# Kernel optimization log

Hardware: AMD Instinct MI355X
Metric: run time of the kernel (lower is better)

Reference implementation:

```python
import jax, jax.numpy as jnp
import numpy as np


def setup_inputs() -> dict:
    key = jax.random.key(0)
    k1, k2 = jax.random.split(key)
    B, D = 8192, 256
    pred = jax.random.normal(k1, (B, D), dtype=jnp.float32)
    gt = jax.random.normal(k2, (B, D), dtype=jnp.float32)
    sigma = jnp.ones((), dtype=jnp.float32)  # learned scalar param (dim=1, mode='auto')
    return {"pred": pred, "gt": gt, "sigma": sigma}


def reference(pred, gt, sigma):
    # p, g: [B, D] (flatten from start_dim=1 is identity for 2D inputs)
    p = pred.reshape(pred.shape[0], -1)
    g = gt.reshape(gt.shape[0], -1)
    B, D = p.shape
    noise_var = sigma ** 2
    # MVN(mean=p_i, cov=noise_var*I).log_prob(g_j) in closed form:
    # -0.5 * ||g_j - p_i||^2 / noise_var - 0.5 * D * log(2*pi*noise_var)
    sq_dist = (
        jnp.sum(p * p, axis=-1)[:, None]
        + jnp.sum(g * g, axis=-1)[None, :]
        - 2.0 * (p @ g.T)
    )  # [B, B]
    log_norm = 0.5 * D * jnp.log(2.0 * jnp.pi * noise_var)
    logits = -0.5 * sq_dist / noise_var - log_norm  # [B, B], class dim = 1
    # cross_entropy(logits, arange(B)) = mean_i(-log_softmax(logits)[i, i])
    logp = jax.nn.log_softmax(logits, axis=1)
    loss = -jnp.mean(jnp.diagonal(logp))
    loss = loss * jax.lax.stop_gradient(2.0 * noise_var)
    return loss
```

## Files before the change

kernel.cpp:

```cpp
#include <hip/hip_runtime.h>
#include <hip/hip_fp8.h>


typedef float f32x4 __attribute__((ext_vector_type(4)));
typedef long llong2 __attribute__((ext_vector_type(2)));

#define LN2F 0.6931471805599453f
#define LOG2EF 1.4426950408889634f
#define NB 8192
#define ND 256
#define NCHUNK 32

#define AS1 __attribute__((address_space(1)))
#define AS3 __attribute__((address_space(3)))

__device__ __forceinline__ float fexp2(float x) {
#if __has_builtin(__builtin_amdgcn_exp2f)
  return __builtin_amdgcn_exp2f(x);
#else
  float r;
  asm("v_exp_f32 %0, %1\n\ts_nop 1" : "=v"(r) : "v"(x));
  return r;
#endif
}

__device__ __forceinline__ int pack4_fp8(float a, float b, float c, float d) {
#if __has_builtin(__builtin_amdgcn_cvt_pk_fp8_f32)
  int w = __builtin_amdgcn_cvt_pk_fp8_f32(a, b, 0, false);
  w = __builtin_amdgcn_cvt_pk_fp8_f32(c, d, w, true);
  return w;
#else
  unsigned b0 = __hip_fp8_e4m3(a).__x, b1 = __hip_fp8_e4m3(b).__x;
  unsigned b2 = __hip_fp8_e4m3(c).__x, b3 = __hip_fp8_e4m3(d).__x;
  return (int)(b0 | (b1 << 8) | (b2 << 16) | (b3 << 24));
#endif
}

__global__ __launch_bounds__(256) void vmse_prep(
    const float* __restrict__ pred, const float* __restrict__ gt,
    const float* __restrict__ sigma,
    unsigned char* __restrict__ Ah, unsigned char* __restrict__ Bh,
    float* __restrict__ diag, float* __restrict__ gnorm,
    float* __restrict__ ghs)
{
  const float nv = sigma[0] * sigma[0];
  const float s = LOG2EF / nv;
  const int row = blockIdx.x * 4 + (threadIdx.x >> 6);
  const int l = threadIdx.x & 63;
  const float4 p = *(const float4*)(pred + row * ND + l * 4);
  const float4 g = *(const float4*)(gt   + row * ND + l * 4);
  const int pw = pack4_fp8(p.x * s, p.y * s, p.z * s, p.w * s);
  const int gw = pack4_fp8(g.x, g.y, g.z, g.w);
  const int pos = (l >> 4) * 64 + ((l & 7) >> 1) * 16 + ((l >> 3) & 1) * 8 + (l & 1) * 4;
  *(int*)(Ah + row * ND + pos) = pw;
  *(int*)(Bh + row * ND + pos) = gw;
  float dd = p.x * g.x + p.y * g.y + p.z * g.z + p.w * g.w;
  float gg = g.x * g.x + g.y * g.y + g.z * g.z + g.w * g.w;
  #pragma unroll
  for (int off = 1; off < 64; off <<= 1) {
    dd += __shfl_xor(dd, off);
    gg += __shfl_xor(gg, off);
  }
  if (l == 0) {
    diag[row] = dd;
    gnorm[row] = gg;
    ghs[row] = -0.5f * s * gg;
  }
}

__device__ __forceinline__ void epi(const f32x4 z, float& m, float& l) {
  const float tmax = fmaxf(fmaxf(z[0], z[1]), fmaxf(z[2], z[3]));
  if (__any(tmax > m + 8.0f)) {
    const float nm = fmaxf(m, tmax);
    l *= fexp2(m - nm);
    m = nm;
  }
  l += (fexp2(z[0] - m) + fexp2(z[1] - m)) + (fexp2(z[2] - m) + fexp2(z[3] - m));
}

__global__ __launch_bounds__(256, 4) void vmse_main(
    const unsigned char* __restrict__ Ah, const unsigned char* __restrict__ Bh,
    const float* __restrict__ ghs, float* __restrict__ partial)
{
  __shared__ unsigned char lds[2][32 * 256];
  __shared__ float lds_ghs[256];
  const int tid = threadIdx.x;
  const int lane = tid & 63;
  const int wid = tid >> 6;
  const int rb = blockIdx.x & 63;
  const int ch = blockIdx.x >> 6;
  const int r15 = lane & 15;
  const int hi = lane >> 4;
  const int j0 = ch * 256;

  long pf[2][8];
  #pragma unroll
  for (int ns = 0; ns < 2; ++ns) {
    const unsigned char* prow =
        Ah + (size_t)((rb * 128) + (wid * 32) + (ns * 16) + r15) * ND;
    #pragma unroll
    for (int kk2 = 0; kk2 < 4; ++kk2) {
      const llong2 v = *(const llong2*)(prow + kk2 * 64 + hi * 16);
      pf[ns][2 * kk2] = v[0];
      pf[ns][2 * kk2 + 1] = v[1];
    }
  }

  lds_ghs[tid] = ghs[j0 + tid];

  const int r7 = r15 & 7;
  const int r7lo = r7 & 3, r7hi = r7 >> 2;
  const int h2 = hi ^ r7lo;
  const char* base = (const char*)&lds[0][0] + r15 * 256 + h2 * 16;
  const char* pE = base + r7hi * 64;
  const char* pO = base + 64 - r7hi * 64;

  const unsigned char* srcb[2];
  #pragma unroll
  for (int i = 0; i < 2; ++i) {
    const int q = wid * 2 + i;
    const int r = q * 4 + (lane >> 4);
    const int cg = (lane & 15) ^ (r & 7);
    srcb[i] = Bh + (size_t)(j0 + r) * ND + cg * 16;
  }

  #define STAGE(buf, t)                                                      \
    {                                                                        \
      _Pragma("unroll")                                                      \
      for (int i = 0; i < 2; ++i)                                            \
        __builtin_amdgcn_global_load_lds(                                    \
            (const AS1 unsigned int*)(srcb[i] + (t) * 8192),                 \
            (AS3 unsigned int*)&lds[buf][(wid * 2 + i) * 1024], 16, 0, 0);   \
    }

  float m2[2], l2[2];
  #pragma unroll
  for (int ns = 0; ns < 2; ++ns) { m2[ns] = -3.0e38f; l2[ns] = 0.0f; }

  #define COMPUTE(PE, PO, gp)                                                \
    {                                                                        \
      _Pragma("unroll")                                                      \
      for (int ms = 0; ms < 2; ++ms) {                                       \
        const f32x4 gv = *(const f32x4*)((gp) + ms * 64 + hi * 16);          \
        f32x4 a0 = gv;                                                       \
        f32x4 a1 = gv;                                                       \
        const llong2 gA = *(const llong2*)((PE) + ms * 4096);                \
        const llong2 gB = *(const llong2*)((PO) + ms * 4096);                \
        const llong2 gC = *(const llong2*)((PE) + ms * 4096 + 128);          \
        const llong2 gD = *(const llong2*)((PO) + ms * 4096 + 128);          \
        const long gf[8] = {gA[0], gA[1], gB[0], gB[1],                      \
                            gC[0], gC[1], gD[0], gD[1]};                     \
        __builtin_amdgcn_s_setprio(1);                                       \
        _Pragma("unroll")                                                    \
        for (int kk = 0; kk < 8; ++kk) {                                     \
          a0 = __builtin_amdgcn_mfma_f32_16x16x32_fp8_fp8(gf[kk], pf[0][kk], a0, 0, 0, 0); \
          a1 = __builtin_amdgcn_mfma_f32_16x16x32_fp8_fp8(gf[kk], pf[1][kk], a1, 0, 0, 0); \
        }                                                                    \
        __builtin_amdgcn_s_setprio(0);                                       \
        epi(a0, m2[0], l2[0]);                                               \
        epi(a1, m2[1], l2[1]);                                               \
      }                                                                      \
    }

  STAGE(0, 0);
  __syncthreads();

  const char* gp = (const char*)lds_ghs;
  for (int tt = 0; tt < 4; ++tt) {
    const int t = 2 * tt;
    STAGE(1, t + 1);
    COMPUTE(pE, pO, gp);
    gp += 128;
    __syncthreads();
    if (t + 2 < 8) STAGE(0, t + 2);
    COMPUTE(pE + 8192, pO + 8192, gp);
    gp += 128;
    __syncthreads();
  }

  #pragma unroll
  for (int ns = 0; ns < 2; ++ns) {
    float m = m2[ns], l = l2[ns];
    #pragma unroll
    for (int off = 16; off <= 32; off <<= 1) {
      const float om = __shfl_xor(m, off);
      const float ol = __shfl_xor(l, off);
      const float nm = fmaxf(m, om);
      l = l * fexp2(m - nm) + ol * fexp2(om - nm);
      m = nm;
    }
    if (hi == 0) {
      const int row = rb * 128 + wid * 32 + ns * 16 + r15;
      partial[row * NCHUNK + ch] = m + log2f(l);
    }
  }
}

__global__ __launch_bounds__(256) void vmse_combine(
    const float* __restrict__ partial, const float* __restrict__ diag,
    const float* __restrict__ gnorm, const float* __restrict__ sigma,
    float* __restrict__ bsum)
{
  const int r = blockIdx.x * 256 + threadIdx.x;
  const float nv = sigma[0] * sigma[0];
  float p[NCHUNK];
  float M = -3.0e38f;
  #pragma unroll
  for (int c = 0; c < NCHUNK; ++c) { p[c] = partial[r * NCHUNK + c]; M = fmaxf(M, p[c]); }
  float ssum = 0.f;
  #pragma unroll
  for (int c = 0; c < NCHUNK; ++c) ssum += exp2f(p[c] - M);
  const float lse2 = M + log2f(ssum);
  const float zii = (diag[r] - 0.5f * gnorm[r]) / nv;
  float contrib = LN2F * lse2 - zii;
  #pragma unroll
  for (int off = 1; off < 64; off <<= 1) contrib += __shfl_xor(contrib, off);
  __shared__ float wsum[4];
  if ((threadIdx.x & 63) == 0) wsum[threadIdx.x >> 6] = contrib;
  __syncthreads();
  if (threadIdx.x == 0)
    bsum[blockIdx.x] = (wsum[0] + wsum[1]) + (wsum[2] + wsum[3]);
}

__global__ __launch_bounds__(64) void vmse_final(
    const float* __restrict__ bsum, const float* __restrict__ sigma,
    float* __restrict__ out)
{
  const int lane = threadIdx.x;
  float v = (lane < 32) ? bsum[lane] : 0.f;
  #pragma unroll
  for (int off = 1; off < 64; off <<= 1) v += __shfl_xor(v, off);
  if (lane == 0) {
    const float nv = sigma[0] * sigma[0];
    out[0] = v * (2.0f * nv / (float)NB);
  }
}

extern "C" void kernel_launch(void* const* d_in, const int* in_sizes, int n_in,
                              void* d_out, int out_size, void* d_ws, size_t ws_size,
                              hipStream_t stream)
{
  const float* pred  = (const float*)d_in[0];
  const float* gt    = (const float*)d_in[1];
  const float* sigma = (const float*)d_in[2];
  char* ws = (char*)d_ws;
  unsigned char* Ah = (unsigned char*)(ws);
  unsigned char* Bh = (unsigned char*)(ws + (2u << 20));
  float* gnorm   = (float*)(ws + (4u << 20));
  float* diag    = (float*)(ws + (4u << 20) + (32u << 10));
  float* ghs     = (float*)(ws + (4u << 20) + (64u << 10));
  float* partial = (float*)(ws + (4u << 20) + (96u << 10));
  float* bsum    = (float*)(ws + (4u << 20) + (96u << 10) + (1u << 20));

  vmse_prep<<<NB / 4, 256, 0, stream>>>(pred, gt, sigma, Ah, Bh, diag, gnorm, ghs);
  vmse_main<<<64 * NCHUNK, 256, 0, stream>>>(Ah, Bh, ghs, partial);
  vmse_combine<<<NB / 256, 256, 0, stream>>>(partial, diag, gnorm, sigma, bsum);
  vmse_final<<<1, 64, 0, stream>>>(bsum, sigma, (float*)d_out);
}
```

Measured before the change: 46.82 us.

## Load whole B chunk into LDS upfront with 512-thread blocks covering 256 rows

Each block now has 8 waves and handles 256 A rows instead of 128. It loads the full 256x256 fp8 B tile (64KB) into LDS in one go, and the double-buffered staging loop with its per-step barriers is removed. This halves the grid and doubles reuse of each B tile across rows, which should cut global traffic and synchronization. In exchange, LDS use grows to about 65KB per block, which limits occupancy, and loads no longer overlap with compute.

```diff
diff --git a/kernel.cpp b/kernel.cpp
--- a/kernel.cpp
+++ b/kernel.cpp
@@ -78,26 +78,38 @@
   l += (fexp2(z[0] - m) + fexp2(z[1] - m)) + (fexp2(z[2] - m) + fexp2(z[3] - m));
 }
 
-__global__ __launch_bounds__(256, 4) void vmse_main(
+__global__ __launch_bounds__(512, 4) void vmse_main(
     const unsigned char* __restrict__ Ah, const unsigned char* __restrict__ Bh,
     const float* __restrict__ ghs, float* __restrict__ partial)
 {
-  __shared__ unsigned char lds[2][32 * 256];
+  __shared__ unsigned char lds[8][32 * 256];
   __shared__ float lds_ghs[256];
   const int tid = threadIdx.x;
   const int lane = tid & 63;
   const int wid = tid >> 6;
-  const int rb = blockIdx.x & 63;
-  const int ch = blockIdx.x >> 6;
+  const int rb = blockIdx.x & 31;
+  const int ch = blockIdx.x >> 5;
   const int r15 = lane & 15;
   const int hi = lane >> 4;
   const int j0 = ch * 256;
 
+  {
+    const int r = wid * 4 + (lane >> 4);
+    const int cg = (lane & 15) ^ (r & 7);
+    const unsigned char* src = Bh + (size_t)(j0 + r) * ND + cg * 16;
+    #pragma unroll
+    for (int t = 0; t < 8; ++t)
+      __builtin_amdgcn_global_load_lds(
+          (const AS1 unsigned int*)(src + t * 8192),
+          (AS3 unsigned int*)&lds[t][wid * 1024], 16, 0, 0);
+  }
+  if (tid < 256) lds_ghs[tid] = ghs[j0 + tid];
+
   long pf[2][8];
   #pragma unroll
   for (int ns = 0; ns < 2; ++ns) {
     const unsigned char* prow =
-        Ah + (size_t)((rb * 128) + (wid * 32) + (ns * 16) + r15) * ND;
+        Ah + (size_t)((rb * 256) + (wid * 32) + (ns * 16) + r15) * ND;
     #pragma unroll
     for (int kk2 = 0; kk2 < 4; ++kk2) {
       const llong2 v = *(const llong2*)(prow + kk2 * 64 + hi * 16);
@@ -105,8 +117,6 @@
       pf[ns][2 * kk2 + 1] = v[1];
     }
   }
-
-  lds_ghs[tid] = ghs[j0 + tid];
 
   const int r7 = r15 & 7;
   const int r7lo = r7 & 3, r7hi = r7 >> 2;
@@ -114,24 +124,6 @@
   const char* base = (const char*)&lds[0][0] + r15 * 256 + h2 * 16;
   const char* pE = base + r7hi * 64;
   const char* pO = base + 64 - r7hi * 64;
-
-  const unsigned char* srcb[2];
-  #pragma unroll
-  for (int i = 0; i < 2; ++i) {
-    const int q = wid * 2 + i;
-    const int r = q * 4 + (lane >> 4);
-    const int cg = (lane & 15) ^ (r & 7);
-    srcb[i] = Bh + (size_t)(j0 + r) * ND + cg * 16;
-  }
-
-  #define STAGE(buf, t)                                                      \
-    {                                                                        \
-      _Pragma("unroll")                                                      \
-      for (int i = 0; i < 2; ++i)                                            \
-        __builtin_amdgcn_global_load_lds(                                    \
-            (const AS1 unsigned int*)(srcb[i] + (t) * 8192),                 \
-            (AS3 unsigned int*)&lds[buf][(wid * 2 + i) * 1024], 16, 0, 0);   \
-    }
 
   float m2[2], l2[2];
   #pragma unroll
@@ -162,20 +154,15 @@
       }                                                                      \
     }
 
-  STAGE(0, 0);
   __syncthreads();
 
+  const char* pEc = pE;
+  const char* pOc = pO;
   const char* gp = (const char*)lds_ghs;
   for (int tt = 0; tt < 4; ++tt) {
-    const int t = 2 * tt;
-    STAGE(1, t + 1);
-    COMPUTE(pE, pO, gp);
-    gp += 128;
-    __syncthreads();
-    if (t + 2 < 8) STAGE(0, t + 2);
-    COMPUTE(pE + 8192, pO + 8192, gp);
-    gp += 128;
-    __syncthreads();
+    COMPUTE(pEc, pOc, gp);
+    COMPUTE(pEc + 8192, pOc + 8192, gp + 128);
+    pEc += 16384; pOc += 16384; gp += 256;
   }
 
   #pragma unroll
@@ -190,7 +177,7 @@
       m = nm;
     }
     if (hi == 0) {
-      const int row = rb * 128 + wid * 32 + ns * 16 + r15;
+      const int row = rb * 256 + wid * 32 + ns * 16 + r15;
       partial[row * NCHUNK + ch] = m + log2f(l);
     }
   }
@@ -253,7 +240,7 @@
   float* bsum    = (float*)(ws + (4u << 20) + (96u << 10) + (1u << 20));
 
   vmse_prep<<<NB / 4, 256, 0, stream>>>(pred, gt, sigma, Ah, Bh, diag, gnorm, ghs);
-  vmse_main<<<64 * NCHUNK, 256, 0, stream>>>(Ah, Bh, ghs, partial);
+  vmse_main<<<32 * NCHUNK, 512, 0, stream>>>(Ah, Bh, ghs, partial);
   vmse_combine<<<NB / 256, 256, 0, stream>>>(partial, diag, gnorm, sigma, bsum);
   vmse_final<<<1, 64, 0, stream>>>(bsum, sigma, (float*)d_out);
 }
```

New measurement: 45.26 us. 3.3% less time.
